# Optimization experiments

Measured on AMD Instinct MI355X. Metric: run time of the kernel, lower is better.

## Reference

```python
import jax, jax.numpy as jnp
import numpy as np

N, E, F_IN, H, D = 50000, 800000, 128, 4, 32


def setup_inputs() -> dict:
    key = jax.random.key(0)
    k1, k2, k3, k4 = jax.random.split(key, 4)
    feat = jax.random.normal(k1, (N, F_IN), dtype=jnp.float32)
    src = jax.random.randint(k2, (E,), 0, N, dtype=jnp.int64)
    dst = jax.random.randint(k3, (E,), 0, N, dtype=jnp.int64)
    # fc weight (xavier-normal-ish scale) and explicit bias
    W = jax.random.normal(k4, (F_IN, H * D), dtype=jnp.float32) * (1.0 / np.sqrt(F_IN))
    bias = jnp.zeros((H * D,), dtype=jnp.float32)
    return {"feat": feat, "src": src, "dst": dst, "W": W, "bias": bias}


def reference(feat, src, dst, W, bias):
    # fc projection, view as (N, H, D)
    ft = (feat @ W).reshape(N, H, D)
    # apply_edges u_dot_v: per-edge per-head dot product -> [E, H]
    e = jnp.einsum("ehd,ehd->eh", ft[src], ft[dst])
    # edge_softmax over incoming edges of each dst node (numerically stable)
    emax = jax.ops.segment_max(e, dst, num_segments=N)  # [N, H]
    ex = jnp.exp(e - emax[dst])
    denom = jax.ops.segment_sum(ex, dst, num_segments=N)  # [N, H]
    a = ex / denom[dst]  # [E, H]
    # update_all: u_mul_e + sum -> weighted scatter aggregation
    msg = ft[src] * a[:, :, None]  # [E, H, D]
    rst = jax.ops.segment_sum(msg, dst, num_segments=N)  # [N, H, D]
    return rst + bias.reshape(1, H, D)
```

## Files before the change

kernel.cpp:

```cpp
#include <hip/hip_runtime.h>
#include <math.h>

#define F 128
#define HEADS 4
#define DHEAD 32
#define HIST_H 128
#define CW_MAX 6592

typedef unsigned short ushort_t;
typedef __attribute__((ext_vector_type(8))) short short8;
typedef __attribute__((ext_vector_type(4))) float f32x4;

__device__ __forceinline__ ushort_t f2bf(float x) {
  unsigned u = __float_as_uint(x);
  unsigned r = u + 0x7FFFu + ((u >> 16) & 1u);
  return (ushort_t)(r >> 16);
}

__device__ __forceinline__ void unpack8(const int4& r, float* v) {
  int rr[4] = {r.x, r.y, r.z, r.w};
#pragma unroll
  for (int q = 0; q < 4; q++) {
    unsigned u = (unsigned)rr[q];
    v[2 * q] = __uint_as_float(u << 16);
    v[2 * q + 1] = __uint_as_float(u & 0xFFFF0000u);
  }
}

__global__ __launch_bounds__(256) void wprep_kernel(
    const float* __restrict__ W, ushort_t* __restrict__ whi,
    ushort_t* __restrict__ wlo) {
  int idx = blockIdx.x * 256 + threadIdx.x;
  if (idx >= 128 * 128) return;
  int j = idx & 7;
  int lane = (idx >> 3) & 63;
  int f = idx >> 9;
  int kt = f >> 3, nt = f & 7;
  int k = kt * 32 + (lane >> 4) * 8 + j;
  int n = nt * 16 + (lane & 15);
  float w = W[k * 128 + n];
  unsigned u = __float_as_uint(w);
  unsigned hb = u & 0xFFFF0000u;
  float lo = w - __uint_as_float(hb);
  whi[idx] = (ushort_t)(hb >> 16);
  wlo[idx] = f2bf(lo);
}

__global__ __launch_bounds__(256) void gemm_kernel(
    const float* __restrict__ feat, const ushort_t* __restrict__ whi,
    const ushort_t* __restrict__ wlo, ushort_t* __restrict__ ftb, int N) {
  const int t = threadIdx.x;
  const int wv = t >> 6;
  const int l = t & 63;
  const int g = l >> 4;
  const int lm = l & 15;
  const int arow = blockIdx.x * 64 + wv * 16 + lm;
  const int arowc = min(arow, N - 1);

  f32x4 acc[8];
#pragma unroll
  for (int nt = 0; nt < 8; nt++) acc[nt] = (f32x4){0.f, 0.f, 0.f, 0.f};

#pragma unroll
  for (int kt = 0; kt < 4; kt++) {
    const float* ap = feat + (size_t)arowc * F + kt * 32 + g * 8;
    float a[8];
    *(float4*)&a[0] = *(const float4*)ap;
    *(float4*)&a[4] = *(const float4*)(ap + 4);
    short8 ahi, alo;
#pragma unroll
    for (int j = 0; j < 8; j++) {
      unsigned u = __float_as_uint(a[j]);
      unsigned hb2 = u & 0xFFFF0000u;
      float lo = a[j] - __uint_as_float(hb2);
      ahi[j] = (short)(hb2 >> 16);
      alo[j] = (short)f2bf(lo);
    }
    const ushort_t* bh = whi + (size_t)(kt * 8) * 512 + l * 8;
    const ushort_t* bl = wlo + (size_t)(kt * 8) * 512 + l * 8;
#pragma unroll
    for (int nt = 0; nt < 8; nt++) {
      short8 bhi = *(const short8*)(bh + nt * 512);
      short8 blo = *(const short8*)(bl + nt * 512);
      acc[nt] =
          __builtin_amdgcn_mfma_f32_16x16x32_bf16(ahi, blo, acc[nt], 0, 0, 0);
      acc[nt] =
          __builtin_amdgcn_mfma_f32_16x16x32_bf16(alo, bhi, acc[nt], 0, 0, 0);
      acc[nt] =
          __builtin_amdgcn_mfma_f32_16x16x32_bf16(ahi, bhi, acc[nt], 0, 0, 0);
    }
  }

  const int orow0 = blockIdx.x * 64 + wv * 16 + g * 4;
#pragma unroll
  for (int reg = 0; reg < 4; reg++) {
    int orow = orow0 + reg;
    if (orow < N) {
#pragma unroll
      for (int nt = 0; nt < 8; nt++)
        ftb[(size_t)orow * F + nt * 16 + lm] = f2bf(acc[nt][reg]);
    }
  }
}

__global__ __launch_bounds__(256) void hist_kernel(
    const int* __restrict__ dst, int* __restrict__ partials, int cwp, int E,
    int N) {
  __shared__ int lh[CW_MAX];
  const int cls = blockIdx.x & 7;
  const int h = blockIdx.x >> 3;
  const int cw = (N + 7) >> 3;
  const int nbase = cls * cw;
  for (int j = threadIdx.x; j < cw; j += 256) lh[j] = 0;
  __syncthreads();
  const int seg = (E + HIST_H - 1) / HIST_H;
  const int e0 = h * seg;
  const int e1 = min(e0 + seg, E);
  int e = e0 + (int)threadIdx.x;
  for (; e + 768 < e1; e += 1024) {
    int d0 = dst[e];
    int d1 = dst[e + 256];
    int d2 = dst[e + 512];
    int d3 = dst[e + 768];
    if ((unsigned)(d0 - nbase) < (unsigned)cw) atomicAdd(&lh[d0 - nbase], 1);
    if ((unsigned)(d1 - nbase) < (unsigned)cw) atomicAdd(&lh[d1 - nbase], 1);
    if ((unsigned)(d2 - nbase) < (unsigned)cw) atomicAdd(&lh[d2 - nbase], 1);
    if ((unsigned)(d3 - nbase) < (unsigned)cw) atomicAdd(&lh[d3 - nbase], 1);
  }
  for (; e < e1; e += 256) {
    int d = dst[e];
    if ((unsigned)(d - nbase) < (unsigned)cw) atomicAdd(&lh[d - nbase], 1);
  }
  __syncthreads();
  int* prow = partials + (size_t)(cls * HIST_H + h) * cwp;
  for (int j = threadIdx.x; j < cw; j += 256) prow[j] = lh[j];
}

__global__ void scan_block_kernel(const int* __restrict__ partials, int cwp,
                                  int* __restrict__ counts,
                                  int* __restrict__ offs,
                                  int* __restrict__ bsums, int N) {
  __shared__ int s[256];
  int t = threadIdx.x, i = blockIdx.x * 256 + t;
  int v = 0;
  if (i < N) {
    int cw = (N + 7) >> 3;
    int c = i / cw;
    int j = i - c * cw;
    const int* base = partials + (size_t)c * HIST_H * cwp + j;
#pragma unroll 8
    for (int h = 0; h < HIST_H; h++) v += base[(size_t)h * cwp];
    counts[i] = v;
  }
  s[t] = v;
  __syncthreads();
  for (int d = 1; d < 256; d <<= 1) {
    int x = (t >= d) ? s[t - d] : 0;
    __syncthreads();
    s[t] += x;
    __syncthreads();
  }
  if (i < N) offs[i] = s[t] - v;
  if (t == 255) bsums[blockIdx.x] = s[255];
}

__global__ void scan_finish_kernel(int* __restrict__ offs,
                                   const int* __restrict__ bsums,
                                   const int* __restrict__ partials,
                                   int* __restrict__ cursors, int cwp, int N) {
  int t = threadIdx.x, b = blockIdx.x;
  int v = (t < b) ? bsums[t] : 0;
#pragma unroll
  for (int d = 32; d > 0; d >>= 1) v += __shfl_down(v, d, 64);
  __shared__ int wsum[4];
  if ((t & 63) == 0) wsum[t >> 6] = v;
  __syncthreads();
  int total = wsum[0] + wsum[1] + wsum[2] + wsum[3];
  int i = b * 256 + t;
  if (i < N) {
    int o = offs[i] + total;
    offs[i] = o;
    int cw = (N + 7) >> 3;
    int c = i / cw;
    int j = i - c * cw;
    const int* pb = partials + (size_t)c * HIST_H * cwp + j;
    int* cb = cursors + (size_t)c * HIST_H * cwp + j;
    int run = o;
#pragma unroll 8
    for (int h = 0; h < HIST_H; h++) {
      cb[(size_t)h * cwp] = run;
      run += pb[(size_t)h * cwp];
    }
  }
}

__global__ __launch_bounds__(256) void scatter_kernel(
    const int* __restrict__ src, const int* __restrict__ dst,
    const int* __restrict__ cursors, int cwp, int* __restrict__ csr, int E,
    int N) {
  __shared__ int lcur[CW_MAX];
  const int cls = blockIdx.x & 7;
  const int h = blockIdx.x >> 3;
  const int cw = (N + 7) >> 3;
  const int nbase = cls * cw;
  const int* crow = cursors + (size_t)(cls * HIST_H + h) * cwp;
  for (int j = threadIdx.x; j < cw; j += 256) lcur[j] = crow[j];
  __syncthreads();
  const int seg = (E + HIST_H - 1) / HIST_H;
  const int e0 = h * seg;
  const int e1 = min(e0 + seg, E);
  int e = e0 + (int)threadIdx.x;
  for (; e + 768 < e1; e += 1024) {
    int d0 = dst[e];
    int d1 = dst[e + 256];
    int d2 = dst[e + 512];
    int d3 = dst[e + 768];
    int s0 = src[e];
    int s1 = src[e + 256];
    int s2 = src[e + 512];
    int s3 = src[e + 768];
    if ((unsigned)(d0 - nbase) < (unsigned)cw)
      csr[atomicAdd(&lcur[d0 - nbase], 1)] = s0;
    if ((unsigned)(d1 - nbase) < (unsigned)cw)
      csr[atomicAdd(&lcur[d1 - nbase], 1)] = s1;
    if ((unsigned)(d2 - nbase) < (unsigned)cw)
      csr[atomicAdd(&lcur[d2 - nbase], 1)] = s2;
    if ((unsigned)(d3 - nbase) < (unsigned)cw)
      csr[atomicAdd(&lcur[d3 - nbase], 1)] = s3;
  }
  for (; e < e1; e += 256) {
    int d = dst[e];
    int sv = src[e];
    if ((unsigned)(d - nbase) < (unsigned)cw)
      csr[atomicAdd(&lcur[d - nbase], 1)] = sv;
  }
}

__global__ __launch_bounds__(256) void aggregate_kernel(
    const ushort_t* __restrict__ ftb, const int* __restrict__ offs,
    const int* __restrict__ counts, const int* __restrict__ csr,
    const float* __restrict__ bias, float* __restrict__ out, int N) {
  const int T = blockIdx.x * 256 + threadIdx.x;
  if (T >= N * 16) return;
  const int sub = T & 3;
  const int p = T >> 2;
  const int h = p & 3;
  const int n = p >> 2;
  const int dimBase = h * DHEAD + sub * 8;

  const int deg = counts[n];
  const int off = offs[n];

  float ftd[8];
  {
    int4 r = *(const int4*)&ftb[n * F + dimBase];
    unpack8(r, ftd);
  }

  const float LOG2E = 1.4426950408889634f;
  float m = -INFINITY, s = 0.f;
  float acc[8];
#pragma unroll
  for (int j = 0; j < 8; j++) acc[j] = 0.f;

#define PROCESS(RX)                                              \
  do {                                                           \
    float v[8];                                                  \
    unpack8(RX, v);                                              \
    float part = 0.f;                                            \
    _Pragma("unroll") for (int j = 0; j < 8; j++) part =         \
        fmaf(ftd[j], v[j], part);                                \
    part += __shfl_xor(part, 1, 4);                              \
    part += __shfl_xor(part, 2, 4);                              \
    float el = part * LOG2E;                                     \
    float mn = fmaxf(m, el);                                     \
    float scale = exp2f(m - mn);                                 \
    float w = exp2f(el - mn);                                    \
    s = fmaf(s, scale, w);                                       \
    _Pragma("unroll") for (int j = 0; j < 8; j++) acc[j] =       \
        fmaf(acc[j], scale, w * v[j]);                           \
    m = mn;                                                      \
  } while (0)

  int4 R0 = make_int4(0, 0, 0, 0), R1 = R0, R2 = R0, R3 = R0;
  if (deg > 0) {
    int dm1 = deg - 1;
    int s0 = csr[off];
    int s1 = csr[off + min(1, dm1)];
    int s2 = csr[off + min(2, dm1)];
    int s3 = csr[off + min(3, dm1)];
    R0 = *(const int4*)&ftb[s0 * F + dimBase];
    R1 = *(const int4*)&ftb[s1 * F + dimBase];
    R2 = *(const int4*)&ftb[s2 * F + dimBase];
    R3 = *(const int4*)&ftb[s3 * F + dimBase];
  }
  int i = 0;
  for (; i + 4 <= deg; i += 4) {
    int dm1 = deg - 1;
    int sa = csr[off + min(i + 4, dm1)];
    int sb = csr[off + min(i + 5, dm1)];
    int sc = csr[off + min(i + 6, dm1)];
    int sd = csr[off + min(i + 7, dm1)];
    int4 Na = *(const int4*)&ftb[sa * F + dimBase];
    int4 Nb = *(const int4*)&ftb[sb * F + dimBase];
    int4 Nc = *(const int4*)&ftb[sc * F + dimBase];
    int4 Nd = *(const int4*)&ftb[sd * F + dimBase];
    PROCESS(R0);
    PROCESS(R1);
    PROCESS(R2);
    PROCESS(R3);
    R0 = Na; R1 = Nb; R2 = Nc; R3 = Nd;
  }
  int r = deg - i;
  if (r > 0) PROCESS(R0);
  if (r > 1) PROCESS(R1);
  if (r > 2) PROCESS(R2);
#undef PROCESS

  float inv = (deg > 0) ? 1.f / s : 0.f;
#pragma unroll
  for (int j = 0; j < 8; j++)
    out[n * F + dimBase + j] = acc[j] * inv + bias[dimBase + j];
}

extern "C" void kernel_launch(void* const* d_in, const int* in_sizes, int n_in,
                              void* d_out, int out_size, void* d_ws,
                              size_t ws_size, hipStream_t stream) {
  const float* feat = (const float*)d_in[0];
  const int* src = (const int*)d_in[1];
  const int* dst = (const int*)d_in[2];
  const float* W = (const float*)d_in[3];
  const float* bias = (const float*)d_in[4];
  float* out = (float*)d_out;

  const int N = in_sizes[0] / F;
  const int E = in_sizes[1];
  const int cw = (N + 7) >> 3;
  const int cwp = (cw + 15) & ~15;

  char* ws = (char*)d_ws;
  ushort_t* ftb = (ushort_t*)ws;
  size_t ftB = (size_t)N * F * sizeof(ushort_t);
  ftB = (ftB + 255) & ~(size_t)255;
  int* counts = (int*)(ws + ftB);
  int* offs = counts + N;
  int* bsums = offs + N;
  int* csr = bsums + 256;
  ushort_t* whi = (ushort_t*)(csr + E);
  ushort_t* wlo = whi + 128 * 128;
  int* partials = (int*)(wlo + 128 * 128);
  int* cursors = partials + 8 * HIST_H * cwp;

  wprep_kernel<<<64, 256, 0, stream>>>(W, whi, wlo);

  gemm_kernel<<<(N + 63) / 64, 256, 0, stream>>>(feat, whi, wlo, ftb, N);

  hist_kernel<<<8 * HIST_H, 256, 0, stream>>>(dst, partials, cwp, E, N);

  int nb = (N + 255) / 256;
  scan_block_kernel<<<nb, 256, 0, stream>>>(partials, cwp, counts, offs,
                                            bsums, N);
  scan_finish_kernel<<<nb, 256, 0, stream>>>(offs, bsums, partials, cursors,
                                             cwp, N);

  scatter_kernel<<<8 * HIST_H, 256, 0, stream>>>(src, dst, cursors, cwp, csr,
                                                 E, N);

  aggregate_kernel<<<(N * 16 + 255) / 256, 256, 0, stream>>>(
      ftb, offs, counts, csr, bias, out, N);
}
```

Baseline: 105.5 us.

## Fuse GEMM with dst histogram and shrink histogram partials to 16-bit

Merges the feature-projection GEMM and the per-chunk dst histogram into one launch, with extra blocks doing the histogram so both run concurrently. The histogram partials and per-chunk cursors are now stored as 16-bit relative counts, and scatter adds them to the global offsets itself. This halves the partial/cursor traffic in the scan and scatter stages. The aggregate epilogue also switches to float4 bias loads and output stores. Risks: the GEMM blocks now reserve the histogram's large shared array, which can lower occupancy, and 16-bit counts overflow if one edge segment sends more than 65535 edges to a single node.

```diff
diff --git a/kernel.cpp b/kernel.cpp
--- a/kernel.cpp
+++ b/kernel.cpp
@@ -46,9 +46,43 @@
   wlo[idx] = f2bf(lo);
 }
 
-__global__ __launch_bounds__(256) void gemm_kernel(
+__global__ __launch_bounds__(256) void gemm_hist_kernel(
     const float* __restrict__ feat, const ushort_t* __restrict__ whi,
-    const ushort_t* __restrict__ wlo, ushort_t* __restrict__ ftb, int N) {
+    const ushort_t* __restrict__ wlo, ushort_t* __restrict__ ftb, int N,
+    const int* __restrict__ dst, ushort_t* __restrict__ partials, int cwp,
+    int E, int gemmBlocks) {
+  __shared__ int lh[CW_MAX];
+  if ((int)blockIdx.x >= gemmBlocks) {
+    const int hb = blockIdx.x - gemmBlocks;
+    const int cls = hb & 7;
+    const int h = hb >> 3;
+    const int cw = (N + 7) >> 3;
+    const int nbase = cls * cw;
+    for (int j = threadIdx.x; j < cw; j += 256) lh[j] = 0;
+    __syncthreads();
+    const int seg = (E + HIST_H - 1) / HIST_H;
+    const int e0 = h * seg;
+    const int e1 = min(e0 + seg, E);
+    int e = e0 + (int)threadIdx.x;
+    for (; e + 768 < e1; e += 1024) {
+      int d0 = dst[e];
+      int d1 = dst[e + 256];
+      int d2 = dst[e + 512];
+      int d3 = dst[e + 768];
+      if ((unsigned)(d0 - nbase) < (unsigned)cw) atomicAdd(&lh[d0 - nbase], 1);
+      if ((unsigned)(d1 - nbase) < (unsigned)cw) atomicAdd(&lh[d1 - nbase], 1);
+      if ((unsigned)(d2 - nbase) < (unsigned)cw) atomicAdd(&lh[d2 - nbase], 1);
+      if ((unsigned)(d3 - nbase) < (unsigned)cw) atomicAdd(&lh[d3 - nbase], 1);
+    }
+    for (; e < e1; e += 256) {
+      int d = dst[e];
+      if ((unsigned)(d - nbase) < (unsigned)cw) atomicAdd(&lh[d - nbase], 1);
+    }
+    __syncthreads();
+    ushort_t* prow = partials + (size_t)(cls * HIST_H + h) * cwp;
+    for (int j = threadIdx.x; j < cw; j += 256) prow[j] = (ushort_t)lh[j];
+    return;
+  }
   const int t = threadIdx.x;
   const int wv = t >> 6;
   const int l = t & 63;
@@ -103,41 +137,8 @@
   }
 }
 
-__global__ __launch_bounds__(256) void hist_kernel(
-    const int* __restrict__ dst, int* __restrict__ partials, int cwp, int E,
-    int N) {
-  __shared__ int lh[CW_MAX];
-  const int cls = blockIdx.x & 7;
-  const int h = blockIdx.x >> 3;
-  const int cw = (N + 7) >> 3;
-  const int nbase = cls * cw;
-  for (int j = threadIdx.x; j < cw; j += 256) lh[j] = 0;
-  __syncthreads();
-  const int seg = (E + HIST_H - 1) / HIST_H;
-  const int e0 = h * seg;
-  const int e1 = min(e0 + seg, E);
-  int e = e0 + (int)threadIdx.x;
-  for (; e + 768 < e1; e += 1024) {
-    int d0 = dst[e];
-    int d1 = dst[e + 256];
-    int d2 = dst[e + 512];
-    int d3 = dst[e + 768];
-    if ((unsigned)(d0 - nbase) < (unsigned)cw) atomicAdd(&lh[d0 - nbase], 1);
-    if ((unsigned)(d1 - nbase) < (unsigned)cw) atomicAdd(&lh[d1 - nbase], 1);
-    if ((unsigned)(d2 - nbase) < (unsigned)cw) atomicAdd(&lh[d2 - nbase], 1);
-    if ((unsigned)(d3 - nbase) < (unsigned)cw) atomicAdd(&lh[d3 - nbase], 1);
-  }
-  for (; e < e1; e += 256) {
-    int d = dst[e];
-    if ((unsigned)(d - nbase) < (unsigned)cw) atomicAdd(&lh[d - nbase], 1);
-  }
-  __syncthreads();
-  int* prow = partials + (size_t)(cls * HIST_H + h) * cwp;
-  for (int j = threadIdx.x; j < cw; j += 256) prow[j] = lh[j];
-}
-
-__global__ void scan_block_kernel(const int* __restrict__ partials, int cwp,
-                                  int* __restrict__ counts,
+__global__ void scan_block_kernel(const ushort_t* __restrict__ partials,
+                                  int cwp, int* __restrict__ counts,
                                   int* __restrict__ offs,
                                   int* __restrict__ bsums, int N) {
   __shared__ int s[256];
@@ -147,7 +148,7 @@
     int cw = (N + 7) >> 3;
     int c = i / cw;
     int j = i - c * cw;
-    const int* base = partials + (size_t)c * HIST_H * cwp + j;
+    const ushort_t* base = partials + (size_t)c * HIST_H * cwp + j;
 #pragma unroll 8
     for (int h = 0; h < HIST_H; h++) v += base[(size_t)h * cwp];
     counts[i] = v;
@@ -166,8 +167,9 @@
 
 __global__ void scan_finish_kernel(int* __restrict__ offs,
                                    const int* __restrict__ bsums,
-                                   const int* __restrict__ partials,
-                                   int* __restrict__ cursors, int cwp, int N) {
+                                   const ushort_t* __restrict__ partials,
+                                   ushort_t* __restrict__ rel16, int cwp,
+                                   int N) {
   int t = threadIdx.x, b = blockIdx.x;
   int v = (t < b) ? bsums[t] : 0;
 #pragma unroll
@@ -178,17 +180,16 @@
   int total = wsum[0] + wsum[1] + wsum[2] + wsum[3];
   int i = b * 256 + t;
   if (i < N) {
-    int o = offs[i] + total;
-    offs[i] = o;
+    offs[i] += total;
     int cw = (N + 7) >> 3;
     int c = i / cw;
     int j = i - c * cw;
-    const int* pb = partials + (size_t)c * HIST_H * cwp + j;
-    int* cb = cursors + (size_t)c * HIST_H * cwp + j;
-    int run = o;
+    const ushort_t* pb = partials + (size_t)c * HIST_H * cwp + j;
+    ushort_t* cb = rel16 + (size_t)c * HIST_H * cwp + j;
+    int run = 0;
 #pragma unroll 8
     for (int h = 0; h < HIST_H; h++) {
-      cb[(size_t)h * cwp] = run;
+      cb[(size_t)h * cwp] = (ushort_t)run;
       run += pb[(size_t)h * cwp];
     }
   }
@@ -196,15 +197,17 @@
 
 __global__ __launch_bounds__(256) void scatter_kernel(
     const int* __restrict__ src, const int* __restrict__ dst,
-    const int* __restrict__ cursors, int cwp, int* __restrict__ csr, int E,
-    int N) {
+    const int* __restrict__ offs, const ushort_t* __restrict__ rel16, int cwp,
+    int* __restrict__ csr, int E, int N) {
   __shared__ int lcur[CW_MAX];
   const int cls = blockIdx.x & 7;
   const int h = blockIdx.x >> 3;
   const int cw = (N + 7) >> 3;
   const int nbase = cls * cw;
-  const int* crow = cursors + (size_t)(cls * HIST_H + h) * cwp;
-  for (int j = threadIdx.x; j < cw; j += 256) lcur[j] = crow[j];
+  const int jmax = min(cw, N - nbase);
+  const ushort_t* crow = rel16 + (size_t)(cls * HIST_H + h) * cwp;
+  for (int j = threadIdx.x; j < jmax; j += 256)
+    lcur[j] = offs[nbase + j] + (int)crow[j];
   __syncthreads();
   const int seg = (E + HIST_H - 1) / HIST_H;
   const int e0 = h * seg;
@@ -318,9 +321,14 @@
 #undef PROCESS
 
   float inv = (deg > 0) ? 1.f / s : 0.f;
-#pragma unroll
-  for (int j = 0; j < 8; j++)
-    out[n * F + dimBase + j] = acc[j] * inv + bias[dimBase + j];
+  float4 b0 = *(const float4*)&bias[dimBase];
+  float4 b1 = *(const float4*)&bias[dimBase + 4];
+  float4 o0 = make_float4(acc[0] * inv + b0.x, acc[1] * inv + b0.y,
+                          acc[2] * inv + b0.z, acc[3] * inv + b0.w);
+  float4 o1 = make_float4(acc[4] * inv + b1.x, acc[5] * inv + b1.y,
+                          acc[6] * inv + b1.z, acc[7] * inv + b1.w);
+  *(float4*)&out[n * F + dimBase] = o0;
+  *(float4*)&out[n * F + dimBase + 4] = o1;
 }
 
 extern "C" void kernel_launch(void* const* d_in, const int* in_sizes, int n_in,
@@ -336,7 +344,7 @@
   const int N = in_sizes[0] / F;
   const int E = in_sizes[1];
   const int cw = (N + 7) >> 3;
-  const int cwp = (cw + 15) & ~15;
+  const int cwp = (cw + 31) & ~31;
 
   char* ws = (char*)d_ws;
   ushort_t* ftb = (ushort_t*)ws;
@@ -348,23 +356,23 @@
   int* csr = bsums + 256;
   ushort_t* whi = (ushort_t*)(csr + E);
   ushort_t* wlo = whi + 128 * 128;
-  int* partials = (int*)(wlo + 128 * 128);
-  int* cursors = partials + 8 * HIST_H * cwp;
+  ushort_t* partials = wlo + 128 * 128;
+  ushort_t* rel16 = partials + 8 * HIST_H * cwp;
 
   wprep_kernel<<<64, 256, 0, stream>>>(W, whi, wlo);
 
-  gemm_kernel<<<(N + 63) / 64, 256, 0, stream>>>(feat, whi, wlo, ftb, N);
-
-  hist_kernel<<<8 * HIST_H, 256, 0, stream>>>(dst, partials, cwp, E, N);
+  int gemmBlocks = (N + 63) / 64;
+  gemm_hist_kernel<<<gemmBlocks + 8 * HIST_H, 256, 0, stream>>>(
+      feat, whi, wlo, ftb, N, dst, partials, cwp, E, gemmBlocks);
 
   int nb = (N + 255) / 256;
   scan_block_kernel<<<nb, 256, 0, stream>>>(partials, cwp, counts, offs,
                                             bsums, N);
-  scan_finish_kernel<<<nb, 256, 0, stream>>>(offs, bsums, partials, cursors,
+  scan_finish_kernel<<<nb, 256, 0, stream>>>(offs, bsums, partials, rel16,
                                              cwp, N);
 
-  scatter_kernel<<<8 * HIST_H, 256, 0, stream>>>(src, dst, cursors, cwp, csr,
-                                                 E, N);
+  scatter_kernel<<<8 * HIST_H, 256, 0, stream>>>(src, dst, offs, rel16, cwp,
+                                                 csr, E, N);
 
   aggregate_kernel<<<(N * 16 + 255) / 256, 256, 0, stream>>>(
       ftb, offs, counts, csr, bias, out, N);
```

Result: faster. 94.45 us (-10.5%).
